# Optimization experiments

Measured on AMD Instinct MI355X. Metric: run time of the kernel, lower is better.

The kernel has to match this reference:

```python
import jax, jax.numpy as jnp
import numpy as np

Q, N, H, C, L = 4, 64, 256, 1, 1024
LOG_TMIN, LOG_TMAX = np.log(0.01), np.log(0.16)


def setup_inputs() -> dict:
    key = jax.random.key(0)
    k0, k1, k2, k3, k4 = jax.random.split(key, 5)
    diagonal = np.log(0.5) + jax.random.normal(k0, (Q, N), dtype=jnp.float32)
    lowrank = jax.random.normal(k1, (Q, N), dtype=jnp.float32)
    timestep = jax.random.uniform(k2, (Q, H), dtype=jnp.float32) * (LOG_TMAX - LOG_TMIN) + LOG_TMIN
    input_matrix = (2.0 * jax.random.uniform(k3, (Q, N), dtype=jnp.float32) - 1.0)  # register(dim=1)
    output_matrix = (2.0 * jax.random.uniform(k4, (Q, C, H, N), dtype=jnp.float32) - 1.0) / np.sqrt(N)
    return {
        'diagonal': diagonal,
        'lowrank': lowrank,
        'timestep': timestep,
        'input_matrix': input_matrix,
        'output_matrix': output_matrix,
        'maxlen': L,
    }


def _get_kernel(diagonal, lowrank, timestep, input_matrix, output_matrix, maxlen):
    # Parameter transforms (as in get_diagonal / get_timestep)
    d = -jnp.exp(diagonal)                      # (Q, N)
    t = jnp.exp(timestep)                       # (Q, H)

    # FFT nodes (setup_omega_z): omega = exp(-2i pi / L) ** arange(L)
    omega0 = jnp.asarray(np.exp(-2j * np.pi / maxlen), dtype=jnp.complex64)
    omega = omega0 ** jnp.arange(maxlen)        # (L,)
    z = 2.0 * (1.0 - omega) / (1.0 + omega)     # bilinear-transform nodes (L,)

    q, n = d.shape
    h = t.shape[1]

    # Stack low-rank term onto B and C channels (get_kernel)
    b = jnp.broadcast_to(input_matrix[:, None, None, :], (q, 1, h, n))
    p = jnp.broadcast_to(lowrank[:, None, None, :], (q, 1, h, n))
    bcat = jnp.concatenate([b, p], axis=1).astype(jnp.complex64)            # (Q, 2, H, N)
    ccat = jnp.concatenate([output_matrix, p], axis=1).astype(jnp.complex64)  # (Q, C+1, H, N)

    # Cauchy resolvent (get_dwoodbury): 1 / (z/t - d), shape (Q, L, H, N)
    zt = jnp.einsum('l,qh->qlh', z, (1.0 / t).astype(jnp.complex64))
    r = 1.0 / (zt[..., None] - d.astype(jnp.complex64)[:, None, None, :])

    # kernel coefficients (compute_slow): (Q, 2, C+1, L, H)
    kcc = jnp.einsum('qihn,qlhn,qchn->qiclh', bcat, r, ccat)

    # Woodbury low-rank correction
    kernel = kcc[:, :-1, :-1] - kcc[:, -1:, :-1] * kcc[:, :-1, -1:] / (1.0 + kcc[:, -1:, -1:])
    kernel = kernel[:, 0]                       # (Q, C, L, H)

    unit = 2.0 / (1.0 + omega)                  # (L,)
    kernel = jnp.einsum('l,qclh->lqch', unit, kernel)  # (L, Q, C, H)

    # inverse real FFT over the frequency axis (crops to L//2+1 bins, like torch)
    kernel = jnp.fft.irfft(kernel, n=maxlen, axis=0)
    return kernel.astype(jnp.float32)           # (L, Q, C, H)


def reference(diagonal, lowrank, timestep, input_matrix, output_matrix, maxlen):
    return _get_kernel(diagonal, lowrank, timestep, input_matrix, output_matrix, maxlen)
```

## Files before the change

kernel.cpp:

```cpp
#include <hip/hip_runtime.h>
#include <math.h>

#define QQ 4
#define NN 64
#define HH 256


typedef float f2 __attribute__((ext_vector_type(2)));

__device__ __forceinline__ float vcos(float rev) { return __builtin_amdgcn_cosf(rev); }
__device__ __forceinline__ float vsin(float rev) { return __builtin_amdgcn_sinf(rev); }

__global__ __launch_bounds__(256)
void tssm_kernel(const float* __restrict__ diagonal,
                 const float* __restrict__ lowrank,
                 const float* __restrict__ timestep,
                 const float* __restrict__ input_matrix,
                 const float* __restrict__ output_matrix,
                 float* __restrict__ out)
{
    __shared__ __align__(16) float2 bufA[512];
    __shared__ __align__(16) float2 bufB[513];
    __shared__ __align__(16) float  sPf[NN * 6];

    const int b  = blockIdx.x;
    const int qh = ((b & 7) << 7) + (b >> 3);
    const int q  = qh >> 8;
    const int t  = threadIdx.x;

    const float tv   = __expf(timestep[qh]);
    const float invt = __builtin_amdgcn_rcpf(tv);

    if (t < NN) {
        float a  = __expf(diagonal[q * NN + t]);
        float B  = input_matrix[q * NN + t];
        float P  = lowrank[q * NN + t];
        float Cm = output_matrix[qh * NN + t];
        float w0 = B * Cm;
        const int base = (t >> 1) * 12 + (t & 1) * 6;
        sPf[base + 0] = a;
        sPf[base + 1] = a * a;
        sPf[base + 2] = w0;
        sPf[base + 3] = B * P;
        sPf[base + 4] = P * Cm;
        sPf[base + 5] = P * P;
        float acc = w0;
        #pragma unroll
        for (int off = 32; off >= 1; off >>= 1) acc += __shfl_xor(acc, off, 64);
        if (t == 0) bufB[512] = make_float2(0.5f * tv * acc, 0.0f);
    }
    __syncthreads();

    const float rv0 = (float)t         * (1.0f / 2048.0f);
    const float rv1 = (float)(t + 256) * (1.0f / 2048.0f);
    const float tn0 = vsin(rv0) * __builtin_amdgcn_rcpf(vcos(rv0));
    const float tn1 = vsin(rv1) * __builtin_amdgcn_rcpf(vcos(rv1));
    const float ze0 = 2.0f * tn0 * invt, ze1 = 2.0f * tn1 * invt;

    const f2 z2v = { ze0 * ze0, ze1 * ze1 };

    f2 r_0 = 0.0f, r_1 = 0.0f, r_2 = 0.0f, r_3 = 0.0f;
    f2 s_0 = 0.0f, s_1 = 0.0f, s_2 = 0.0f, s_3 = 0.0f;

    #define POLE(PA, PA2, PW0, PW1, PW2, PW3)                                \
    {                                                                        \
        f2 d = (PA2) + z2v;                                    \
        f2 g;                                                                \
        g.x = __builtin_amdgcn_rcpf(d.x);                                    \
        g.y = __builtin_amdgcn_rcpf(d.y);                                    \
        f2 ag = (PA) * g;                                      \
        r_0 = __builtin_elementwise_fma((f2)(PW0), ag, r_0);                 \
        s_0 = __builtin_elementwise_fma((f2)(PW0), g,  s_0);                 \
        r_1 = __builtin_elementwise_fma((f2)(PW1), ag, r_1);                 \
        s_1 = __builtin_elementwise_fma((f2)(PW1), g,  s_1);                 \
        r_2 = __builtin_elementwise_fma((f2)(PW2), ag, r_2);                 \
        s_2 = __builtin_elementwise_fma((f2)(PW2), g,  s_2);                 \
        r_3 = __builtin_elementwise_fma((f2)(PW3), ag, r_3);                 \
        s_3 = __builtin_elementwise_fma((f2)(PW3), g,  s_3);                 \
    }

    {
        const float4* __restrict__ T4 = (const float4*)sPf;
        #pragma unroll 4
        for (int p = 0; p < 32; ++p) {
            float4 Av = T4[3 * p];
            float4 Bv = T4[3 * p + 1];
            float4 Cv = T4[3 * p + 2];
            POLE(Av.x, Av.y, Av.z, Av.w, Bv.x, Bv.y)
            POLE(Bv.z, Bv.w, Cv.x, Cv.y, Cv.z, Cv.w)
        }
    }
    #undef POLE

    {
        float i0 = -ze0 * s_0.x, i1 = -ze0 * s_1.x, i2 = -ze0 * s_2.x, i3 = -ze0 * s_3.x;
        float dr = 1.0f + r_3.x, di = i3;
        float nr = r_2.x * r_1.x - i2 * i1;
        float ni = r_2.x * i1 + i2 * r_1.x;
        float invm = __builtin_amdgcn_rcpf(fmaf(dr, dr, di * di));
        float qr = (nr * dr + ni * di) * invm;
        float qi = (ni * dr - nr * di) * invm;
        float Kr = r_0.x - qr, Ki = i0 - qi;
        bufB[t] = make_float2(fmaf(-tn0, Ki, Kr), fmaf(tn0, Kr, Ki));
    }
    {
        float i0 = -ze1 * s_0.y, i1 = -ze1 * s_1.y, i2 = -ze1 * s_2.y, i3 = -ze1 * s_3.y;
        float dr = 1.0f + r_3.y, di = i3;
        float nr = r_2.y * r_1.y - i2 * i1;
        float ni = r_2.y * i1 + i2 * r_1.y;
        float invm = __builtin_amdgcn_rcpf(fmaf(dr, dr, di * di));
        float qr = (nr * dr + ni * di) * invm;
        float qi = (ni * dr - nr * di) * invm;
        float Kr = r_0.y - qr, Ki = i0 - qi;
        bufB[t + 256] = make_float2(fmaf(-tn1, Ki, Kr), fmaf(tn1, Kr, Ki));
    }
    __syncthreads();

    const float c1 = vcos((float)t * 0.0009765625f);
    const float s1 = vsin((float)t * 0.0009765625f);

    float Y0r, Y0i, Y1r, Y1i;
    {
        float2 A = bufB[t], Bv = bufB[512 - t];
        float Dr = A.x - Bv.x, Di = A.y + Bv.y;
        float twDr = fmaf(c1, Dr, -s1 * Di);
        float twDi = fmaf(c1, Di,  s1 * Dr);
        Y0r = 0.5f * (A.x + Bv.x) - 0.5f * twDi;
        Y0i = 0.5f * (A.y - Bv.y) + 0.5f * twDr;
    }
    {
        float2 A = bufB[t + 256], Bv = bufB[256 - t];
        float Dr = A.x - Bv.x, Di = A.y + Bv.y;
        float twDr = fmaf(-s1, Dr, -c1 * Di);
        float twDi = fmaf(-s1, Di,  c1 * Dr);
        Y1r = 0.5f * (A.x + Bv.x) - 0.5f * twDi;
        Y1i = 0.5f * (A.y - Bv.y) + 0.5f * twDr;
    }

    ((float4*)bufA)[t] = make_float4(Y0r + Y1r, Y0i + Y1i, Y0r - Y1r, Y0i - Y1i);
    __syncthreads();

    #define FFT_STAGE(NS, REVNS, SRC, DST)                                   \
    {                                                                        \
        float2 u = (SRC)[t];                                                 \
        float2 v = (SRC)[t + 256];                                           \
        int   base = t & ((NS) - 1);                                         \
        float rev = (float)base * (REVNS);                                   \
        float cw = vcos(rev), sw = vsin(rev);                                \
        float vr = fmaf(cw, v.x, -sw * v.y);                                 \
        float vi = fmaf(cw, v.y,  sw * v.x);                                 \
        int dj = ((t & ~((NS) - 1)) << 1) | base;                            \
        (DST)[dj]        = make_float2(u.x + vr, u.y + vi);                  \
        (DST)[dj + (NS)] = make_float2(u.x - vr, u.y - vi);                  \
        __syncthreads();                                                     \
    }

    FFT_STAGE(2,   0.25f,         bufA, bufB)
    FFT_STAGE(4,   0.125f,        bufB, bufA)
    FFT_STAGE(8,   0.0625f,       bufA, bufB)
    FFT_STAGE(16,  0.03125f,      bufB, bufA)
    FFT_STAGE(32,  0.015625f,     bufA, bufB)
    FFT_STAGE(64,  0.0078125f,    bufB, bufA)
    FFT_STAGE(128, 0.00390625f,   bufA, bufB)
    #undef FFT_STAGE

    {
        float2 u = bufB[t];
        float2 v = bufB[t + 256];
        float rev = (float)t * 0.001953125f;
        float cw = vcos(rev), sw = vsin(rev);
        float vr = fmaf(cw, v.x, -sw * v.y);
        float vi = fmaf(cw, v.y,  sw * v.x);
        const float sc = 1.0f / 512.0f;
        const int s0 = 2 * t;
        out[( s0        << 10) + qh] = (u.x + vr) * sc;
        out[((s0 + 1)   << 10) + qh] = (u.y + vi) * sc;
        out[((s0 + 512) << 10) + qh] = (u.x - vr) * sc;
        out[((s0 + 513) << 10) + qh] = (u.y - vi) * sc;
    }
}

extern "C" void kernel_launch(void* const* d_in, const int* in_sizes, int n_in,
                              void* d_out, int out_size, void* d_ws, size_t ws_size,
                              hipStream_t stream) {
    (void)in_sizes; (void)n_in; (void)out_size; (void)d_ws; (void)ws_size;
    const float* diagonal      = (const float*)d_in[0];
    const float* lowrank       = (const float*)d_in[1];
    const float* timestep      = (const float*)d_in[2];
    const float* input_matrix  = (const float*)d_in[3];
    const float* output_matrix = (const float*)d_in[4];
    float* out = (float*)d_out;

    hipLaunchKernelGGL(tssm_kernel, dim3(QQ * HH), dim3(256), 0, stream,
                       diagonal, lowrank, timestep, input_matrix, output_matrix, out);
}
```

Baseline: 18.12 us.

## Replace radix-2 FFT stages with radix-4 stages to halve barriers

The 512-point complex FFT changes from eight radix-2 Stockham stages to four radix-4 stages, each computed by 128 threads handling four points. This cuts the number of shared-memory passes and __syncthreads barriers roughly in half. In exchange, half the threads sit idle during the FFT and each active thread does more twiddle sin/cos evaluations. The output stage now writes eight values per active thread.

```diff
diff --git a/kernel.cpp b/kernel.cpp
--- a/kernel.cpp
+++ b/kernel.cpp
@@ -64,11 +64,11 @@
 
     #define POLE(PA, PA2, PW0, PW1, PW2, PW3)                                \
     {                                                                        \
-        f2 d = (PA2) + z2v;                                    \
+        f2 d = (PA2) + z2v;                                                  \
         f2 g;                                                                \
         g.x = __builtin_amdgcn_rcpf(d.x);                                    \
         g.y = __builtin_amdgcn_rcpf(d.y);                                    \
-        f2 ag = (PA) * g;                                      \
+        f2 ag = (PA) * g;                                                    \
         r_0 = __builtin_elementwise_fma((f2)(PW0), ag, r_0);                 \
         s_0 = __builtin_elementwise_fma((f2)(PW0), g,  s_0);                 \
         r_1 = __builtin_elementwise_fma((f2)(PW1), ag, r_1);                 \
@@ -140,43 +140,66 @@
     ((float4*)bufA)[t] = make_float4(Y0r + Y1r, Y0i + Y1i, Y0r - Y1r, Y0i - Y1i);
     __syncthreads();
 
-    #define FFT_STAGE(NS, REVNS, SRC, DST)                                   \
-    {                                                                        \
-        float2 u = (SRC)[t];                                                 \
-        float2 v = (SRC)[t + 256];                                           \
-        int   base = t & ((NS) - 1);                                         \
-        float rev = (float)base * (REVNS);                                   \
-        float cw = vcos(rev), sw = vsin(rev);                                \
-        float vr = fmaf(cw, v.x, -sw * v.y);                                 \
-        float vi = fmaf(cw, v.y,  sw * v.x);                                 \
-        int dj = ((t & ~((NS) - 1)) << 1) | base;                            \
-        (DST)[dj]        = make_float2(u.x + vr, u.y + vi);                  \
-        (DST)[dj + (NS)] = make_float2(u.x - vr, u.y - vi);                  \
-        __syncthreads();                                                     \
-    }
-
-    FFT_STAGE(2,   0.25f,         bufA, bufB)
-    FFT_STAGE(4,   0.125f,        bufB, bufA)
-    FFT_STAGE(8,   0.0625f,       bufA, bufB)
-    FFT_STAGE(16,  0.03125f,      bufB, bufA)
-    FFT_STAGE(32,  0.015625f,     bufA, bufB)
-    FFT_STAGE(64,  0.0078125f,    bufB, bufA)
-    FFT_STAGE(128, 0.00390625f,   bufA, bufB)
-    #undef FFT_STAGE
-
-    {
-        float2 u = bufB[t];
-        float2 v = bufB[t + 256];
+    #define FFT_STAGE4(NS, REVNS, SRC, DST)                                   \
+    if (t < 128) {                                                            \
+        int base = t & ((NS) - 1);                                            \
+        int blk  = t / (NS);                                                  \
+        float2 u0 = (SRC)[t],       u1 = (SRC)[t + 128];                      \
+        float2 u2 = (SRC)[t + 256], u3 = (SRC)[t + 384];                      \
+        float rev = (float)base * (REVNS);                                    \
+        float c1v = vcos(rev),          s1w = vsin(rev);                      \
+        float c2v = vcos(2.0f * rev),   s2w = vsin(2.0f * rev);               \
+        float c3v = vcos(3.0f * rev),   s3w = vsin(3.0f * rev);               \
+        float v1r = fmaf(c1v, u1.x, -s1w * u1.y);                             \
+        float v1i = fmaf(c1v, u1.y,  s1w * u1.x);                             \
+        float v2r = fmaf(c2v, u2.x, -s2w * u2.y);                             \
+        float v2i = fmaf(c2v, u2.y,  s2w * u2.x);                             \
+        float v3r = fmaf(c3v, u3.x, -s3w * u3.y);                             \
+        float v3i = fmaf(c3v, u3.y,  s3w * u3.x);                             \
+        float ar = u0.x + v2r, ai = u0.y + v2i;                               \
+        float br = u0.x - v2r, bi = u0.y - v2i;                               \
+        float cr = v1r + v3r,  ci = v1i + v3i;                                \
+        float dr2 = v1r - v3r, di2 = v1i - v3i;                               \
+        int dj = blk * (4 * (NS)) + base;                                     \
+        (DST)[dj]            = make_float2(ar + cr,  ai + ci);                \
+        (DST)[dj + (NS)]     = make_float2(br - di2, bi + dr2);               \
+        (DST)[dj + 2*(NS)]   = make_float2(ar - cr,  ai - ci);                \
+        (DST)[dj + 3*(NS)]   = make_float2(br + di2, bi - dr2);               \
+    }                                                                         \
+    __syncthreads();
+
+    FFT_STAGE4(2,  0.125f,      bufA, bufB)
+    FFT_STAGE4(8,  0.03125f,    bufB, bufA)
+    FFT_STAGE4(32, 0.0078125f,  bufA, bufB)
+    #undef FFT_STAGE4
+
+    if (t < 128) {
+        float2 u0 = bufB[t],       u1 = bufB[t + 128];
+        float2 u2 = bufB[t + 256], u3 = bufB[t + 384];
         float rev = (float)t * 0.001953125f;
-        float cw = vcos(rev), sw = vsin(rev);
-        float vr = fmaf(cw, v.x, -sw * v.y);
-        float vi = fmaf(cw, v.y,  sw * v.x);
+        float c1v = vcos(rev),          s1w = vsin(rev);
+        float c2v = vcos(2.0f * rev),   s2w = vsin(2.0f * rev);
+        float c3v = vcos(3.0f * rev),   s3w = vsin(3.0f * rev);
+        float v1r = fmaf(c1v, u1.x, -s1w * u1.y);
+        float v1i = fmaf(c1v, u1.y,  s1w * u1.x);
+        float v2r = fmaf(c2v, u2.x, -s2w * u2.y);
+        float v2i = fmaf(c2v, u2.y,  s2w * u2.x);
+        float v3r = fmaf(c3v, u3.x, -s3w * u3.y);
+        float v3i = fmaf(c3v, u3.y,  s3w * u3.x);
+        float ar = u0.x + v2r, ai = u0.y + v2i;
+        float br = u0.x - v2r, bi = u0.y - v2i;
+        float cr = v1r + v3r,  ci = v1i + v3i;
+        float dr2 = v1r - v3r, di2 = v1i - v3i;
         const float sc = 1.0f / 512.0f;
         const int s0 = 2 * t;
-        out[( s0        << 10) + qh] = (u.x + vr) * sc;
-        out[((s0 + 1)   << 10) + qh] = (u.y + vi) * sc;
-        out[((s0 + 512) << 10) + qh] = (u.x - vr) * sc;
-        out[((s0 + 513) << 10) + qh] = (u.y - vi) * sc;
+        out[( s0          << 10) + qh] = (ar + cr)  * sc;
+        out[((s0 + 1)     << 10) + qh] = (ai + ci)  * sc;
+        out[((s0 + 256)   << 10) + qh] = (br - di2) * sc;
+        out[((s0 + 257)   << 10) + qh] = (bi + dr2) * sc;
+        out[((s0 + 512)   << 10) + qh] = (ar - cr)  * sc;
+        out[((s0 + 513)   << 10) + qh] = (ai - ci)  * sc;
+        out[((s0 + 768)   << 10) + qh] = (br + di2) * sc;
+        out[((s0 + 769)   << 10) + qh] = (bi - dr2) * sc;
     }
 }
 
```

Result: no change. 18.15 us (+0.2%).
